# Kernel tuning notes

Hardware: AMD Instinct MI355X
Metric: run time of the kernel (lower is better)

## Reference

```python
import jax, jax.numpy as jnp
import numpy as np

NGRAM_NS = (2, 3)  # window sizes of the 2 hidden layers ('2,3,4' -> num_hidden_layers=2)


def _ngram(x, n):
    # x: (b, s, d) -> (b, s, n, d); window i holds x[i:i+n], zero-padded at the end
    s = x.shape[1]
    xp = jnp.pad(x, ((0, 0), (0, n - 1), (0, 0)))
    return jnp.stack([xp[:, j:j + s] for j in range(n)], axis=2)


def _mixture_weighted(r, i, w):
    # r,i: (..., n, d); w: (..., n, 1) -> weighted sum of outer products |phi><phi|
    w = w[..., 0]
    Rr = jnp.einsum('...nd,...ne,...n->...de', r, r, w) + jnp.einsum('...nd,...ne,...n->...de', i, i, w)
    Ri = jnp.einsum('...nd,...ne,...n->...de', i, r, w) - jnp.einsum('...nd,...ne,...n->...de', r, i, w)
    return Rr, Ri


def _normalize_complex(vr, vi):
    n = jnp.sqrt(jnp.sum(vr * vr + vi * vi, axis=-1, keepdims=True))
    return vr / n, vi / n


def _quad_form(Rr, Ri, vr, vi):
    # <v_k| rho |v_k> for each measurement vector v_k; Rr,Ri: (..., d, d); vr,vi: (k, d)
    ar = jnp.einsum('...de,ke->...dk', Rr, vr) - jnp.einsum('...de,ke->...dk', Ri, vi)
    ai = jnp.einsum('...de,ke->...dk', Rr, vi) + jnp.einsum('...de,ke->...dk', Ri, vr)
    out_r = jnp.einsum('kd,...dk->...k', vr, ar) + jnp.einsum('kd,...dk->...k', vi, ai)
    out_i = jnp.einsum('kd,...dk->...k', vr, ai) - jnp.einsum('kd,...dk->...k', vi, ar)
    return out_r, out_i


def setup_inputs() -> dict:
    key = jax.random.key(0)
    ks = jax.random.split(key, 9)
    V, D, B, S, U, L = 50000, 100, 16, 128, 100, 2
    return {
        'input_seq': jax.random.randint(ks[0], (B, S), 0, V),
        'amp_table': jax.random.normal(ks[1], (V, D), jnp.float32),
        'phase_table': jax.random.uniform(ks[2], (V, D), jnp.float32, -np.pi, np.pi),
        'proj_kernel_r': jax.random.normal(ks[3], (L, D, D), jnp.float32),
        'proj_kernel_i': jax.random.normal(ks[4], (L, D, D), jnp.float32),
        'meas_kernel_r': jax.random.normal(ks[5], (U, D), jnp.float32),
        'meas_kernel_i': jax.random.normal(ks[6], (U, D), jnp.float32),
        'dense_w': jax.random.normal(ks[7], (U, 2), jnp.float32) * 0.1,
        'dense_b': jnp.zeros((2,), jnp.float32),
    }


def reference(input_seq, amp_table, phase_table, proj_kernel_r, proj_kernel_i,
              meas_kernel_r, meas_kernel_i, dense_w, dense_b):
    # ComplexEmbedding
    amp = amp_table[input_seq]      # (b, s, d)
    phase = phase_table[input_seq]  # (b, s, d)
    # L2Norm / L2Normalization
    weights = jnp.linalg.norm(amp, axis=-1, keepdims=True)  # (b, s, 1)
    amp = amp / weights
    # ComplexMultiply: state = amp * e^{i phase}
    seq_r = amp * jnp.cos(phase)
    seq_i = amp * jnp.sin(phase)
    for li, n in enumerate(NGRAM_NS):
        gr = _ngram(seq_r, n)                                  # (b, s, n, d)
        gi = _ngram(seq_i, n)
        gw = jax.nn.softmax(_ngram(weights, n), axis=1)        # Softmax(dim=1) as in torch code
        Rr, Ri = _mixture_weighted(gr, gi, gw)                 # (b, s, d, d)
        vr, vi = _normalize_complex(proj_kernel_r[li], proj_kernel_i[li])
        seq_r, seq_i = _quad_form(Rr, Ri, vr, vi)              # (b, s, d)
    # Final mixture over the sequence dim with the raw L2-norm weights
    Rr, Ri = _mixture_weighted(seq_r, seq_i, weights)          # (b, d, d)
    vr, vi = _normalize_complex(meas_kernel_r, meas_kernel_i)
    probs, _ = _quad_form(Rr, Ri, vr, vi)                      # (b, units) real part of Tr(rho P_k)
    return probs @ dense_w + dense_b
```

## Files before the change

### kernel.cpp

```cpp
#include <hip/hip_runtime.h>
#include <math.h>

#define NB 16
#define SS 128
#define DD 100
#define KK 100
#define T_TILE 8
#define P_HALO 11
#define NTILES 16
#define NT 768
#define NWAVES 12
#define CH_D4 5
#define NCHUNK 5

template<int MODE>
__device__ __forceinline__ void accum_slot(
    const float4* __restrict__ vtb,
    const float4 (*__restrict__ bxr)[25], const float4 (*__restrict__ bxi)[25],
    int p, int k, int c, float& ar, float& ai)
{
#pragma unroll
  for (int r = 0; r < CH_D4; ++r) {
    const int d4 = c * CH_D4 + r;
    const float4 vr4 = vtb[r * KK + k];
    const float4 vi4 = vtb[500 + r * KK + k];
    const float4 x4  = bxr[p][d4];
    if (MODE == 0) {
      const float4 z4 = bxi[p][d4];
      ar += vr4.x * x4.x + vr4.y * x4.y + vr4.z * x4.z + vr4.w * x4.w
          + vi4.x * z4.x + vi4.y * z4.y + vi4.z * z4.z + vi4.w * z4.w;
      ai += vr4.x * z4.x + vr4.y * z4.y + vr4.z * z4.z + vr4.w * z4.w
          - vi4.x * x4.x - vi4.y * x4.y - vi4.z * x4.z - vi4.w * x4.w;
    } else {
      ar += vr4.x * x4.x + vr4.y * x4.y + vr4.z * x4.z + vr4.w * x4.w;
      ai += vi4.x * x4.x + vi4.y * x4.y + vi4.z * x4.z + vi4.w * x4.w;
    }
  }
}

template<int MODE>
__device__ __forceinline__ void run_stage(
    const float* __restrict__ gvr, const float* __restrict__ gvi,
    float4 (*__restrict__ vt)[1000],
    const float4 (*__restrict__ bxr)[25], const float4 (*__restrict__ bxi)[25],
    float* __restrict__ mflat, float2* __restrict__ y2flat,
    float* __restrict__ invvn, const int nslots,
    const int tid, const int lane, const int wid)
{
  if (tid < 4 * KK) {
    const int k = tid >> 2, q = tid & 3;
    const float* r0 = gvr + k * DD + q;
    const float* i0 = gvi + k * DD + q;
    float s = 0.f;
#pragma unroll
    for (int i = 0; i < 25; ++i) { const float a = r0[4*i], c2 = i0[4*i]; s += a*a + c2*c2; }
    s += __shfl_xor(s, 1, 64);
    s += __shfl_xor(s, 2, 64);
    if (q == 0) invvn[k] = 1.0f / s;
  }

  const int e0 = tid;
  const int e1 = tid + NT;
  const int p0 = e0 / 500, rm0 = e0 % 500, r0_ = rm0 / 100, k0_ = rm0 % 100;
  const int p1 = e1 / 500, rm1 = e1 % 500, r1_ = rm1 / 100, k1_ = rm1 % 100;
  const float* g0 = (p0 ? gvi : gvr) + k0_ * DD + 4 * r0_;
  const float* g1 = (p1 ? gvi : gvr) + k1_ * DD + 4 * r1_;

  float4 pv0, pv1;
  pv0 = *(const float4*)(g0);
  if (e1 < 1000) pv1 = *(const float4*)(g1);
  vt[0][e0] = pv0;
  if (e1 < 1000) vt[0][e1] = pv1;
  __syncthreads();

  const int s0 = wid, s1 = wid + NWAVES;
  float a0r = 0.f, a0i = 0.f, a1r = 0.f, a1i = 0.f;
  const int kk0 = (s0 & 1) * 50 + lane;
  const int kk1 = (s1 & 1) * 50 + lane;
  const int pp0 = s0 >> 1, pp1 = s1 >> 1;

  for (int c = 0; c < NCHUNK; ++c) {
    const int buf = c & 1;
    if (c + 1 < NCHUNK) {
      pv0 = *(const float4*)(g0 + 4 * CH_D4 * (c + 1));
      if (e1 < 1000) pv1 = *(const float4*)(g1 + 4 * CH_D4 * (c + 1));
    }
    if (lane < 50) {
      if (s0 < nslots) accum_slot<MODE>(vt[buf], bxr, bxi, pp0, kk0, c, a0r, a0i);
      if (s1 < nslots) accum_slot<MODE>(vt[buf], bxr, bxi, pp1, kk1, c, a1r, a1i);
    }
    if (c + 1 < NCHUNK) {
      const int nb = buf ^ 1;
      vt[nb][e0] = pv0;
      if (e1 < 1000) vt[nb][e1] = pv1;
    }
    __syncthreads();
  }

  if (lane < 50) {
    if (s0 < nslots) {
      if (MODE == 0) mflat[pp0 * KK + kk0] = (a0r * a0r + a0i * a0i) * invvn[kk0];
      else           y2flat[pp0 * KK + kk0] = make_float2(a0r, a0i);
    }
    if (s1 < nslots) {
      if (MODE == 0) mflat[pp1 * KK + kk1] = (a1r * a1r + a1i * a1i) * invvn[kk1];
      else           y2flat[pp1 * KK + kk1] = make_float2(a1r, a1i);
    }
  }
}

__global__ __launch_bounds__(NT) void k_fused(
    const int* __restrict__ seq,
    const float* __restrict__ ampT, const float* __restrict__ phT,
    const float* __restrict__ pkr, const float* __restrict__ pki,
    const float* __restrict__ mkr, const float* __restrict__ mki,
    float* __restrict__ part)
{
  __shared__ float4 vt[2][1000];
  __shared__ float4 xr4[P_HALO][25];
  __shared__ float4 xi4[P_HALO][25];
  __shared__ float4 m4[P_HALO][25];
  __shared__ float2 y2[P_HALO][KK];
  __shared__ float es[SS];
  __shared__ float wnl[SS];
  __shared__ float invvn[KK];
  __shared__ float redw[NWAVES];
  __shared__ float sc[3];

  const int tid  = threadIdx.x;
  const int lane = tid & 63;
  const int wid  = tid >> 6;
  const int bt   = blockIdx.x;
  const int b    = bt >> 4;
  const int tile = bt & 15;
  const int t0   = tile * T_TILE;
  const int sb   = b * SS;

  if (tid < 4 * SS) {
    const int t = tid >> 2, q = tid & 3;
    const int row = seq[sb + t];
    const float* ap = ampT + (long)row * DD + q;
    float s = 0.f;
#pragma unroll
    for (int i = 0; i < 25; ++i) { const float a = ap[4*i]; s += a * a; }
    s += __shfl_xor(s, 1, 64);
    s += __shfl_xor(s, 2, 64);
    if (q == 0) { const float nrm = sqrtf(s); wnl[t] = nrm; es[t] = expf(nrm); }
  }
  __syncthreads();

  {
    float v = (tid < SS) ? es[tid] : 0.f;
    for (int m = 32; m; m >>= 1) v += __shfl_xor(v, m, 64);
    if (lane == 0) redw[wid] = v;
  }
  for (int idx = tid; idx < P_HALO * 25; idx += NT) {
    const int p = idx / 25, d4 = idx % 25;
    const int tp = t0 + p;
    float4 o_r = {0.f, 0.f, 0.f, 0.f}, o_i = {0.f, 0.f, 0.f, 0.f};
    if (tp < SS) {
      const int row = seq[sb + tp];
      const float4 a4 = *(const float4*)(ampT + (long)row * DD + 4 * d4);
      const float4 p4 = *(const float4*)(phT  + (long)row * DD + 4 * d4);
      const float inv = 1.0f / wnl[tp];
      float sv, cv;
      sincosf(p4.x, &sv, &cv); o_r.x = a4.x * inv * cv; o_i.x = a4.x * inv * sv;
      sincosf(p4.y, &sv, &cv); o_r.y = a4.y * inv * cv; o_i.y = a4.y * inv * sv;
      sincosf(p4.z, &sv, &cv); o_r.z = a4.z * inv * cv; o_i.z = a4.z * inv * sv;
      sincosf(p4.w, &sv, &cv); o_r.w = a4.w * inv * cv; o_i.w = a4.w * inv * sv;
    }
    xr4[p][d4] = o_r;
    xi4[p][d4] = o_i;
  }
  __syncthreads();
  if (tid == 0) {
    float E = 0.f;
    for (int w = 0; w < NWAVES; ++w) E += redw[w];
    sc[0] = E;
    sc[1] = E - es[0] + 1.0f;
    sc[2] = E - es[0] - es[1] + 2.0f;
  }
  __syncthreads();

  run_stage<0>(pkr, pki, vt, xr4, xi4, (float*)m4, nullptr, invvn,
               2 * P_HALO, tid, lane, wid);
  __syncthreads();

  run_stage<1>(pkr + DD * DD, pki + DD * DD, vt, m4, m4, nullptr,
               (float2*)y2, invvn, 2 * P_HALO, tid, lane, wid);
  __syncthreads();

  {
    const float E = sc[0], Z1 = sc[1];
    for (int idx = tid; idx < 10 * KK; idx += NT) {
      const int p = idx / KK, k = idx - p * KK;
      const int t = t0 + p;
      const float w0 = ((t     < SS) ? es[t]     : 1.f) / E;
      const float w1 = ((t + 1 < SS) ? es[t + 1] : 1.f) / Z1;
      const float2 ya = y2[p][k], yb = y2[p + 1][k];
      const float ar = w0 * ya.x + w1 * yb.x;
      const float ai = w0 * ya.y + w1 * yb.y;
      ((float*)m4)[p * KK + k] = (ar * ar + ai * ai) * invvn[k];
    }
  }
  __syncthreads();

  run_stage<1>(mkr, mki, vt, m4, m4, nullptr,
               (float2*)y2, invvn, 20, tid, lane, wid);
  __syncthreads();

  {
    const float E = sc[0], Z1 = sc[1], Z2 = sc[2];
    for (int idx = tid; idx < T_TILE * KK; idx += NT) {
      const int p = idx / KK, k = idx - p * KK;
      const int t = t0 + p;
      const float w0 = es[t] / E;
      const float w1 = ((t + 1 < SS) ? es[t + 1] : 1.f) / Z1;
      const float w2 = ((t + 2 < SS) ? es[t + 2] : 1.f) / Z2;
      const float2 ya = y2[p][k], yb = y2[p + 1][k], yc = y2[p + 2][k];
      const float qr = w0 * ya.x + w1 * yb.x + w2 * yc.x;
      const float qi = w0 * ya.y + w1 * yb.y + w2 * yc.y;
      ((float*)m4)[p * KK + k] = wnl[t] * (qr * qr + qi * qi) * invvn[k];
    }
  }
  __syncthreads();
  if (tid < KK) {
    float s = 0.f;
#pragma unroll
    for (int p = 0; p < T_TILE; ++p) s += ((float*)m4)[p * KK + tid];
    part[bt * KK + tid] = s;
  }
}

__global__ __launch_bounds__(128) void k_out(
    const float* __restrict__ part, const float* __restrict__ dw,
    const float* __restrict__ db, float* __restrict__ out)
{
  __shared__ float pr[KK];
  const int b = blockIdx.x, tid = threadIdx.x;
  if (tid < KK) {
    float s = 0.f;
#pragma unroll
    for (int q = 0; q < NTILES; ++q) s += part[(b * NTILES + q) * KK + tid];
    pr[tid] = s;
  }
  __syncthreads();
  if (tid < 2) {
    float s = db[tid];
    for (int k = 0; k < KK; ++k) s += pr[k] * dw[k * 2 + tid];
    out[b * 2 + tid] = s;
  }
}

extern "C" void kernel_launch(void* const* d_in, const int* in_sizes, int n_in,
                              void* d_out, int out_size, void* d_ws, size_t ws_size,
                              hipStream_t stream) {
  const int*   seq  = (const int*)d_in[0];
  const float* ampT = (const float*)d_in[1];
  const float* phT  = (const float*)d_in[2];
  const float* pkr  = (const float*)d_in[3];
  const float* pki  = (const float*)d_in[4];
  const float* mkr  = (const float*)d_in[5];
  const float* mki  = (const float*)d_in[6];
  const float* dw   = (const float*)d_in[7];
  const float* db   = (const float*)d_in[8];
  float* out  = (float*)d_out;
  float* part = (float*)d_ws;

  k_fused<<<NB * NTILES, NT, 0, stream>>>(seq, ampT, phT, pkr, pki, mkr, mki, part);
  k_out  <<<NB,          128, 0, stream>>>(part, dw, db, out);
}
```

Baseline: 35.46 us.

## Stage activations in global workspace and read them with wave-uniform scalar loads

Embedded activations and intermediate stage outputs now go to global workspace buffers instead of shared memory. Each wave reads three positions' activation rows through s_load into scalar registers, while lanes hold per-unit vectors from a padded LDS buffer. The projection norm is folded into the accumulation loop, the block shrinks to 512 threads, and the final mixing is reduced straight into the partial sums. The aim is to cut LDS traffic and redundant broadcast reads. In exchange the kernel takes extra global round-trips and relies on scalar-cache visibility of data the same block has just written.

Result: slower. 50.84 us (+43.4%).

```diff
diff --git a/kernel.cpp b/kernel.cpp
--- a/kernel.cpp
+++ b/kernel.cpp
@@ -6,107 +6,157 @@
 #define DD 100
 #define KK 100
 #define T_TILE 8
-#define P_HALO 11
 #define NTILES 16
-#define NT 768
-#define NWAVES 12
-#define CH_D4 5
-#define NCHUNK 5
-
-template<int MODE>
-__device__ __forceinline__ void accum_slot(
-    const float4* __restrict__ vtb,
-    const float4 (*__restrict__ bxr)[25], const float4 (*__restrict__ bxi)[25],
-    int p, int k, int c, float& ar, float& ai)
-{
-#pragma unroll
-  for (int r = 0; r < CH_D4; ++r) {
-    const int d4 = c * CH_D4 + r;
-    const float4 vr4 = vtb[r * KK + k];
-    const float4 vi4 = vtb[500 + r * KK + k];
-    const float4 x4  = bxr[p][d4];
-    if (MODE == 0) {
-      const float4 z4 = bxi[p][d4];
-      ar += vr4.x * x4.x + vr4.y * x4.y + vr4.z * x4.z + vr4.w * x4.w
-          + vi4.x * z4.x + vi4.y * z4.y + vi4.z * z4.z + vi4.w * z4.w;
-      ai += vr4.x * z4.x + vr4.y * z4.y + vr4.z * z4.z + vr4.w * z4.w
-          - vi4.x * x4.x - vi4.y * x4.y - vi4.z * x4.z - vi4.w * x4.w;
-    } else {
-      ar += vr4.x * x4.x + vr4.y * x4.y + vr4.z * x4.z + vr4.w * x4.w;
-      ai += vi4.x * x4.x + vi4.y * x4.y + vi4.z * x4.z + vi4.w * x4.w;
-    }
+#define NT 512
+#define ROWF 112
+#define VSTR 52
+#define VPLANE 5200
+#define XROW(b,t) ((((b) << 7) + (t)) * ROWF)
+
+typedef float sf16 __attribute__((ext_vector_type(16)));
+typedef float sf8  __attribute__((ext_vector_type(8)));
+typedef float sf4  __attribute__((ext_vector_type(4)));
+
+__device__ __forceinline__ sf16 sl16(const float* p) {
+  sf16 r; asm volatile("s_load_dwordx16 %0, %1, 0x0" : "=s"(r) : "s"((unsigned long long)p)); return r;
+}
+__device__ __forceinline__ sf8 sl8(const float* p) {
+  sf8 r; asm volatile("s_load_dwordx8 %0, %1, 0x0" : "=s"(r) : "s"((unsigned long long)p)); return r;
+}
+__device__ __forceinline__ sf4 sl4(const float* p) {
+  sf4 r; asm volatile("s_load_dwordx4 %0, %1, 0x0" : "=s"(r) : "s"((unsigned long long)p)); return r;
+}
+
+template<int NF4>
+__device__ __forceinline__ void vload(const float* __restrict__ sr, const float* __restrict__ si,
+                                      int cd, int tid, float4 (&vr)[6]) {
+  const int tot = 2 * KK * NF4;
+#pragma unroll
+  for (int i = 0; i < 6; ++i) {
+    const int e = tid + i * NT;
+    if (e < tot) {
+      const int part = e / (KK * NF4);
+      const int r = e - part * (KK * NF4);
+      const int k = r / NF4;
+      const int j = r - k * NF4;
+      vr[i] = *(const float4*)((part ? si : sr) + k * DD + cd + 4 * j);
+    }
+  }
+}
+template<int NF4>
+__device__ __forceinline__ void vstore(float* __restrict__ vbuf, int tid, const float4 (&vr)[6]) {
+  const int tot = 2 * KK * NF4;
+#pragma unroll
+  for (int i = 0; i < 6; ++i) {
+    const int e = tid + i * NT;
+    if (e < tot) {
+      const int part = e / (KK * NF4);
+      const int r = e - part * (KK * NF4);
+      const int k = r / NF4;
+      const int j = r - k * NF4;
+      *(float4*)&vbuf[part * VPLANE + k * VSTR + 4 * j] = vr[i];
+    }
+  }
+}
+
+#define NRM() nacc += vr.x*vr.x+vr.y*vr.y+vr.z*vr.z+vr.w*vr.w \
+                    + vi.x*vi.x+vi.y*vi.y+vi.z*vi.z+vi.w*vi.w
+#define C0B(AX, BX, P) \
+  ar[P]+=vr.x*AX[4*u+0]+vr.y*AX[4*u+1]+vr.z*AX[4*u+2]+vr.w*AX[4*u+3] \
+       +vi.x*BX[4*u+0]+vi.y*BX[4*u+1]+vi.z*BX[4*u+2]+vi.w*BX[4*u+3]; \
+  ai[P]+=vr.x*BX[4*u+0]+vr.y*BX[4*u+1]+vr.z*BX[4*u+2]+vr.w*BX[4*u+3] \
+       -vi.x*AX[4*u+0]-vi.y*AX[4*u+1]-vi.z*AX[4*u+2]-vi.w*AX[4*u+3];
+#define C1B(AX, P) \
+  ar[P]+=vr.x*AX[4*u+0]+vr.y*AX[4*u+1]+vr.z*AX[4*u+2]+vr.w*AX[4*u+3]; \
+  ai[P]+=vi.x*AX[4*u+0]+vi.y*AX[4*u+1]+vi.z*AX[4*u+2]+vi.w*AX[4*u+3];
+
+template<int ND4>
+__device__ __forceinline__ void fma_c0(const float* __restrict__ vbuf, int ke,
+    const float* xr0, const float* xr1, const float* xr2,
+    const float* xi0, const float* xi1, const float* xi2,
+    int cd, float (&ar)[3], float (&ai)[3], float& nacc) {
+  const float* vb = vbuf + ke * VSTR;
+#pragma unroll 1
+  for (int s = 0; s < ND4 / 2; ++s) {
+    sf8 a0 = sl8(xr0 + cd + 8*s), a1 = sl8(xr1 + cd + 8*s), a2 = sl8(xr2 + cd + 8*s);
+    sf8 b0 = sl8(xi0 + cd + 8*s), b1 = sl8(xi1 + cd + 8*s), b2 = sl8(xi2 + cd + 8*s);
+    asm volatile("s_waitcnt lgkmcnt(0)"
+                 : "+s"(a0), "+s"(a1), "+s"(a2), "+s"(b0), "+s"(b1), "+s"(b2));
+#pragma unroll
+    for (int u = 0; u < 2; ++u) {
+      const float4 vr = *(const float4*)(vb + (2*s+u)*4);
+      const float4 vi = *(const float4*)(vb + VPLANE + (2*s+u)*4);
+      NRM();
+      C0B(a0, b0, 0) C0B(a1, b1, 1) C0B(a2, b2, 2)
+    }
+  }
+  if (ND4 & 1) {
+    const int off = cd + 8 * (ND4 / 2);
+    sf4 a0 = sl4(xr0 + off), a1 = sl4(xr1 + off), a2 = sl4(xr2 + off);
+    sf4 b0 = sl4(xi0 + off), b1 = sl4(xi1 + off), b2 = sl4(xi2 + off);
+    asm volatile("s_waitcnt lgkmcnt(0)"
+                 : "+s"(a0), "+s"(a1), "+s"(a2), "+s"(b0), "+s"(b1), "+s"(b2));
+    const int u = 0;
+    const float4 vr = *(const float4*)(vb + (ND4-1)*4);
+    const float4 vi = *(const float4*)(vb + VPLANE + (ND4-1)*4);
+    NRM();
+    C0B(a0, b0, 0) C0B(a1, b1, 1) C0B(a2, b2, 2)
+  }
+}
+
+template<int ND4>
+__device__ __forceinline__ void fma_c1(const float* __restrict__ vbuf, int ke,
+    const float* x0, const float* x1, const float* x2,
+    int cd, float (&ar)[3], float (&ai)[3], float& nacc) {
+  const float* vb = vbuf + ke * VSTR;
+#pragma unroll 1
+  for (int s = 0; s < ND4 / 4; ++s) {
+    sf16 a0 = sl16(x0 + cd + 16*s), a1 = sl16(x1 + cd + 16*s), a2 = sl16(x2 + cd + 16*s);
+    asm volatile("s_waitcnt lgkmcnt(0)" : "+s"(a0), "+s"(a1), "+s"(a2));
+#pragma unroll
+    for (int u = 0; u < 4; ++u) {
+      const float4 vr = *(const float4*)(vb + (4*s+u)*4);
+      const float4 vi = *(const float4*)(vb + VPLANE + (4*s+u)*4);
+      NRM();
+      C1B(a0, 0) C1B(a1, 1) C1B(a2, 2)
+    }
+  }
+  if (ND4 & 3) {
+    const int off = cd + 16 * (ND4 / 4);
+    sf4 a0 = sl4(x0 + off), a1 = sl4(x1 + off), a2 = sl4(x2 + off);
+    asm volatile("s_waitcnt lgkmcnt(0)" : "+s"(a0), "+s"(a1), "+s"(a2));
+    const int u = 0;
+    const float4 vr = *(const float4*)(vb + (ND4-1)*4);
+    const float4 vi = *(const float4*)(vb + VPLANE + (ND4-1)*4);
+    NRM();
+    C1B(a0, 0) C1B(a1, 1) C1B(a2, 2)
   }
 }
 
 template<int MODE>
 __device__ __forceinline__ void run_stage(
     const float* __restrict__ gvr, const float* __restrict__ gvi,
-    float4 (*__restrict__ vt)[1000],
-    const float4 (*__restrict__ bxr)[25], const float4 (*__restrict__ bxi)[25],
-    float* __restrict__ mflat, float2* __restrict__ y2flat,
-    float* __restrict__ invvn, const int nslots,
-    const int tid, const int lane, const int wid)
-{
-  if (tid < 4 * KK) {
-    const int k = tid >> 2, q = tid & 3;
-    const float* r0 = gvr + k * DD + q;
-    const float* i0 = gvi + k * DD + q;
-    float s = 0.f;
-#pragma unroll
-    for (int i = 0; i < 25; ++i) { const float a = r0[4*i], c2 = i0[4*i]; s += a*a + c2*c2; }
-    s += __shfl_xor(s, 1, 64);
-    s += __shfl_xor(s, 2, 64);
-    if (q == 0) invvn[k] = 1.0f / s;
-  }
-
-  const int e0 = tid;
-  const int e1 = tid + NT;
-  const int p0 = e0 / 500, rm0 = e0 % 500, r0_ = rm0 / 100, k0_ = rm0 % 100;
-  const int p1 = e1 / 500, rm1 = e1 % 500, r1_ = rm1 / 100, k1_ = rm1 % 100;
-  const float* g0 = (p0 ? gvi : gvr) + k0_ * DD + 4 * r0_;
-  const float* g1 = (p1 ? gvi : gvr) + k1_ * DD + 4 * r1_;
-
-  float4 pv0, pv1;
-  pv0 = *(const float4*)(g0);
-  if (e1 < 1000) pv1 = *(const float4*)(g1);
-  vt[0][e0] = pv0;
-  if (e1 < 1000) vt[0][e1] = pv1;
-  __syncthreads();
-
-  const int s0 = wid, s1 = wid + NWAVES;
-  float a0r = 0.f, a0i = 0.f, a1r = 0.f, a1i = 0.f;
-  const int kk0 = (s0 & 1) * 50 + lane;
-  const int kk1 = (s1 & 1) * 50 + lane;
-  const int pp0 = s0 >> 1, pp1 = s1 >> 1;
-
-  for (int c = 0; c < NCHUNK; ++c) {
-    const int buf = c & 1;
-    if (c + 1 < NCHUNK) {
-      pv0 = *(const float4*)(g0 + 4 * CH_D4 * (c + 1));
-      if (e1 < 1000) pv1 = *(const float4*)(g1 + 4 * CH_D4 * (c + 1));
-    }
-    if (lane < 50) {
-      if (s0 < nslots) accum_slot<MODE>(vt[buf], bxr, bxi, pp0, kk0, c, a0r, a0i);
-      if (s1 < nslots) accum_slot<MODE>(vt[buf], bxr, bxi, pp1, kk1, c, a1r, a1i);
-    }
-    if (c + 1 < NCHUNK) {
-      const int nb = buf ^ 1;
-      vt[nb][e0] = pv0;
-      if (e1 < 1000) vt[nb][e1] = pv1;
-    }
-    __syncthreads();
-  }
-
-  if (lane < 50) {
-    if (s0 < nslots) {
-      if (MODE == 0) mflat[pp0 * KK + kk0] = (a0r * a0r + a0i * a0i) * invvn[kk0];
-      else           y2flat[pp0 * KK + kk0] = make_float2(a0r, a0i);
-    }
-    if (s1 < nslots) {
-      if (MODE == 0) mflat[pp1 * KK + kk1] = (a1r * a1r + a1i * a1i) * invvn[kk1];
-      else           y2flat[pp1 * KK + kk1] = make_float2(a1r, a1i);
-    }
-  }
+    const float* xr0, const float* xr1, const float* xr2,
+    const float* xi0, const float* xi1, const float* xi2,
+    float* __restrict__ vbuf, float* __restrict__ invvn,
+    int tid, int ke, bool nwrite, float (&ar)[3], float (&ai)[3]) {
+  float4 vreg[6];
+  ar[0] = ar[1] = ar[2] = 0.f; ai[0] = ai[1] = ai[2] = 0.f;
+  float nacc = 0.f;
+  vload<12>(gvr, gvi, 0, tid, vreg);
+  vstore<12>(vbuf, tid, vreg);
+  __syncthreads();
+  vload<13>(gvr, gvi, 48, tid, vreg);
+  if (MODE == 0) fma_c0<12>(vbuf, ke, xr0, xr1, xr2, xi0, xi1, xi2, 0, ar, ai, nacc);
+  else           fma_c1<12>(vbuf, ke, xr0, xr1, xr2, 0, ar, ai, nacc);
+  __syncthreads();
+  vstore<13>(vbuf, tid, vreg);
+  __syncthreads();
+  if (MODE == 0) fma_c0<13>(vbuf, ke, xr0, xr1, xr2, xi0, xi1, xi2, 48, ar, ai, nacc);
+  else           fma_c1<13>(vbuf, ke, xr0, xr1, xr2, 48, ar, ai, nacc);
+  __syncthreads();
+  if (nwrite) invvn[ke] = 1.0f / nacc;
+  __syncthreads();
 }
 
 __global__ __launch_bounds__(NT) void k_fused(
@@ -114,134 +164,166 @@
     const float* __restrict__ ampT, const float* __restrict__ phT,
     const float* __restrict__ pkr, const float* __restrict__ pki,
     const float* __restrict__ mkr, const float* __restrict__ mki,
-    float* __restrict__ part)
-{
-  __shared__ float4 vt[2][1000];
-  __shared__ float4 xr4[P_HALO][25];
-  __shared__ float4 xi4[P_HALO][25];
-  __shared__ float4 m4[P_HALO][25];
-  __shared__ float2 y2[P_HALO][KK];
-  __shared__ float es[SS];
-  __shared__ float wnl[SS];
-  __shared__ float invvn[KK];
-  __shared__ float redw[NWAVES];
-  __shared__ float sc[3];
+    float* __restrict__ PR, float* __restrict__ PI,
+    float* __restrict__ M1, float* __restrict__ M2,
+    float* __restrict__ part) {
+  __shared__ float vbuf[2 * VPLANE];
+  __shared__ float2 y2l[11 * 102];
+  __shared__ float es[SS], wnl[SS], invvn[KK];
+  __shared__ float redw[2], sc[3];
 
   const int tid  = threadIdx.x;
   const int lane = tid & 63;
-  const int wid  = tid >> 6;
+  const int wid  = __builtin_amdgcn_readfirstlane(tid >> 6);
   const int bt   = blockIdx.x;
   const int b    = bt >> 4;
-  const int tile = bt & 15;
-  const int t0   = tile * T_TILE;
+  const int t0   = (bt & 15) * T_TILE;
   const int sb   = b * SS;
-
-  if (tid < 4 * SS) {
-    const int t = tid >> 2, q = tid & 3;
+  const int q    = wid & 1;
+  const int pg   = wid >> 1;
+  const int ke   = q * 50 + (lane < 50 ? lane : 49);
+  const int pp0 = pg, pp1 = pg + 4, pp2 = pg + 8;
+
+  {
+    const int t = tid >> 2, qq = tid & 3;
     const int row = seq[sb + t];
-    const float* ap = ampT + (long)row * DD + q;
+    const float* ap = ampT + (long)row * DD + qq;
     float s = 0.f;
 #pragma unroll
     for (int i = 0; i < 25; ++i) { const float a = ap[4*i]; s += a * a; }
-    s += __shfl_xor(s, 1, 64);
-    s += __shfl_xor(s, 2, 64);
-    if (q == 0) { const float nrm = sqrtf(s); wnl[t] = nrm; es[t] = expf(nrm); }
-  }
-  __syncthreads();
-
+    s += __shfl_xor(s, 1); s += __shfl_xor(s, 2);
+    if (qq == 0) { const float n = sqrtf(s); wnl[t] = n; es[t] = expf(n); }
+  }
+  __syncthreads();
   {
     float v = (tid < SS) ? es[tid] : 0.f;
-    for (int m = 32; m; m >>= 1) v += __shfl_xor(v, m, 64);
-    if (lane == 0) redw[wid] = v;
-  }
-  for (int idx = tid; idx < P_HALO * 25; idx += NT) {
-    const int p = idx / 25, d4 = idx % 25;
-    const int tp = t0 + p;
-    float4 o_r = {0.f, 0.f, 0.f, 0.f}, o_i = {0.f, 0.f, 0.f, 0.f};
-    if (tp < SS) {
-      const int row = seq[sb + tp];
-      const float4 a4 = *(const float4*)(ampT + (long)row * DD + 4 * d4);
-      const float4 p4 = *(const float4*)(phT  + (long)row * DD + 4 * d4);
-      const float inv = 1.0f / wnl[tp];
-      float sv, cv;
-      sincosf(p4.x, &sv, &cv); o_r.x = a4.x * inv * cv; o_i.x = a4.x * inv * sv;
-      sincosf(p4.y, &sv, &cv); o_r.y = a4.y * inv * cv; o_i.y = a4.y * inv * sv;
-      sincosf(p4.z, &sv, &cv); o_r.z = a4.z * inv * cv; o_i.z = a4.z * inv * sv;
-      sincosf(p4.w, &sv, &cv); o_r.w = a4.w * inv * cv; o_i.w = a4.w * inv * sv;
-    }
-    xr4[p][d4] = o_r;
-    xi4[p][d4] = o_i;
+    if (tid < SS) {
+      for (int m = 32; m; m >>= 1) v += __shfl_xor(v, m);
+      if (lane == 0) redw[tid >> 6] = v;
+    }
+  }
+  for (int e = tid; e < 11 * DD; e += NT) {
+    const int p = e / DD, d = e - p * DD;
+    const int t = t0 + p;
+    if (t < SS) {
+      const int row = seq[sb + t];
+      const float a  = ampT[(long)row * DD + d];
+      const float ph = phT[(long)row * DD + d];
+      float sv, cv; sincosf(ph, &sv, &cv);
+      const float an = a / wnl[t];
+      PR[XROW(b, t) + d] = an * cv;
+      PI[XROW(b, t) + d] = an * sv;
+    }
   }
   __syncthreads();
   if (tid == 0) {
-    float E = 0.f;
-    for (int w = 0; w < NWAVES; ++w) E += redw[w];
-    sc[0] = E;
-    sc[1] = E - es[0] + 1.0f;
-    sc[2] = E - es[0] - es[1] + 2.0f;
-  }
-  __syncthreads();
-
-  run_stage<0>(pkr, pki, vt, xr4, xi4, (float*)m4, nullptr, invvn,
-               2 * P_HALO, tid, lane, wid);
-  __syncthreads();
-
-  run_stage<1>(pkr + DD * DD, pki + DD * DD, vt, m4, m4, nullptr,
-               (float2*)y2, invvn, 2 * P_HALO, tid, lane, wid);
-  __syncthreads();
-
-  {
-    const float E = sc[0], Z1 = sc[1];
+    const float E = redw[0] + redw[1];
+    sc[0] = E; sc[1] = E - es[0] + 1.0f; sc[2] = E - es[0] - es[1] + 2.0f;
+  }
+  __syncthreads();
+
+  float ar[3], ai[3];
+  const bool nwr = (wid < 2) && (lane < 63 ? (lane < 50) : false);
+
+  {
+    const int r0 = min(t0 + min(pp0, 10), SS - 1);
+    const int r1 = min(t0 + min(pp1, 10), SS - 1);
+    const int r2 = min(t0 + min(pp2, 10), SS - 1);
+    run_stage<0>(pkr, pki,
+                 PR + XROW(b, r0), PR + XROW(b, r1), PR + XROW(b, r2),
+                 PI + XROW(b, r0), PI + XROW(b, r1), PI + XROW(b, r2),
+                 vbuf, invvn, tid, ke, nwr, ar, ai);
+#pragma unroll
+    for (int j = 0; j < 3; ++j) {
+      const int pp = pg + 4 * j;
+      const int t = t0 + pp;
+      if (pp < 11 && t < SS && lane < 50)
+        M1[XROW(b, t) + ke] = (ar[j] * ar[j] + ai[j] * ai[j]) * invvn[ke];
+    }
+    __syncthreads();
+  }
+
+  {
+    const int r0 = min(t0 + min(pp0, 10), SS - 1);
+    const int r1 = min(t0 + min(pp1, 10), SS - 1);
+    const int r2 = min(t0 + min(pp2, 10), SS - 1);
+    run_stage<1>(pkr + DD * DD, pki + DD * DD,
+                 M1 + XROW(b, r0), M1 + XROW(b, r1), M1 + XROW(b, r2),
+                 nullptr, nullptr, nullptr,
+                 vbuf, invvn, tid, ke, nwr, ar, ai);
+#pragma unroll
+    for (int j = 0; j < 3; ++j) {
+      const int pp = pg + 4 * j;
+      if (pp < 11 && lane < 50) y2l[pp * 102 + ke] = make_float2(ar[j], ai[j]);
+    }
+    __syncthreads();
     for (int idx = tid; idx < 10 * KK; idx += NT) {
       const int p = idx / KK, k = idx - p * KK;
       const int t = t0 + p;
-      const float w0 = ((t     < SS) ? es[t]     : 1.f) / E;
-      const float w1 = ((t + 1 < SS) ? es[t + 1] : 1.f) / Z1;
-      const float2 ya = y2[p][k], yb = y2[p + 1][k];
-      const float ar = w0 * ya.x + w1 * yb.x;
-      const float ai = w0 * ya.y + w1 * yb.y;
-      ((float*)m4)[p * KK + k] = (ar * ar + ai * ai) * invvn[k];
-    }
-  }
-  __syncthreads();
-
-  run_stage<1>(mkr, mki, vt, m4, m4, nullptr,
-               (float2*)y2, invvn, 20, tid, lane, wid);
-  __syncthreads();
-
-  {
-    const float E = sc[0], Z1 = sc[1], Z2 = sc[2];
-    for (int idx = tid; idx < T_TILE * KK; idx += NT) {
-      const int p = idx / KK, k = idx - p * KK;
-      const int t = t0 + p;
-      const float w0 = es[t] / E;
-      const float w1 = ((t + 1 < SS) ? es[t + 1] : 1.f) / Z1;
-      const float w2 = ((t + 2 < SS) ? es[t + 2] : 1.f) / Z2;
-      const float2 ya = y2[p][k], yb = y2[p + 1][k], yc = y2[p + 2][k];
-      const float qr = w0 * ya.x + w1 * yb.x + w2 * yc.x;
-      const float qi = w0 * ya.y + w1 * yb.y + w2 * yc.y;
-      ((float*)m4)[p * KK + k] = wnl[t] * (qr * qr + qi * qi) * invvn[k];
-    }
-  }
-  __syncthreads();
-  if (tid < KK) {
-    float s = 0.f;
-#pragma unroll
-    for (int p = 0; p < T_TILE; ++p) s += ((float*)m4)[p * KK + tid];
-    part[bt * KK + tid] = s;
+      if (t < SS) {
+        const float w0 = es[t] / sc[0];
+        float qr = w0 * y2l[p * 102 + k].x;
+        float qi = w0 * y2l[p * 102 + k].y;
+        if (t + 1 < SS) {
+          const float w1 = es[t + 1] / sc[1];
+          qr += w1 * y2l[(p + 1) * 102 + k].x;
+          qi += w1 * y2l[(p + 1) * 102 + k].y;
+        }
+        M2[XROW(b, t) + k] = (qr * qr + qi * qi) * invvn[k];
+      }
+    }
+    __syncthreads();
+  }
+
+  {
+    const int r0 = min(t0 + min(pp0, 9), SS - 1);
+    const int r1 = min(t0 + min(pp1, 9), SS - 1);
+    const int r2 = min(t0 + min(pp2, 9), SS - 1);
+    run_stage<1>(mkr, mki,
+                 M2 + XROW(b, r0), M2 + XROW(b, r1), M2 + XROW(b, r2),
+                 nullptr, nullptr, nullptr,
+                 vbuf, invvn, tid, ke, nwr, ar, ai);
+#pragma unroll
+    for (int j = 0; j < 3; ++j) {
+      const int pp = pg + 4 * j;
+      if (pp < 10 && lane < 50) y2l[pp * 102 + ke] = make_float2(ar[j], ai[j]);
+    }
+    __syncthreads();
+    if (tid < KK) {
+      const int k = tid;
+      float accf = 0.f;
+#pragma unroll
+      for (int p = 0; p < T_TILE; ++p) {
+        const int t = t0 + p;
+        const float w0 = es[t] / sc[0];
+        float qr = w0 * y2l[p * 102 + k].x;
+        float qi = w0 * y2l[p * 102 + k].y;
+        if (t + 1 < SS) {
+          const float w1 = es[t + 1] / sc[1];
+          qr += w1 * y2l[(p + 1) * 102 + k].x;
+          qi += w1 * y2l[(p + 1) * 102 + k].y;
+        }
+        if (t + 2 < SS) {
+          const float w2 = es[t + 2] / sc[2];
+          qr += w2 * y2l[(p + 2) * 102 + k].x;
+          qi += w2 * y2l[(p + 2) * 102 + k].y;
+        }
+        accf += wnl[t] * (qr * qr + qi * qi);
+      }
+      part[bt * KK + k] = accf * invvn[k];
+    }
   }
 }
 
 __global__ __launch_bounds__(128) void k_out(
     const float* __restrict__ part, const float* __restrict__ dw,
-    const float* __restrict__ db, float* __restrict__ out)
-{
+    const float* __restrict__ db, float* __restrict__ out) {
   __shared__ float pr[KK];
   const int b = blockIdx.x, tid = threadIdx.x;
   if (tid < KK) {
     float s = 0.f;
 #pragma unroll
-    for (int q = 0; q < NTILES; ++q) s += part[(b * NTILES + q) * KK + tid];
+    for (int qq = 0; qq < NTILES; ++qq) s += part[(b * NTILES + qq) * KK + tid];
     pr[tid] = s;
   }
   __syncthreads();
@@ -264,9 +346,17 @@
   const float* mki  = (const float*)d_in[6];
   const float* dw   = (const float*)d_in[7];
   const float* db   = (const float*)d_in[8];
-  float* out  = (float*)d_out;
-  float* part = (float*)d_ws;
-
-  k_fused<<<NB * NTILES, NT, 0, stream>>>(seq, ampT, phT, pkr, pki, mkr, mki, part);
+  float* out = (float*)d_out;
+
+  float* ws = (float*)d_ws;
+  const int R = NB * SS * ROWF;
+  float* PR   = ws;
+  float* PI   = ws + R;
+  float* M1   = ws + 2 * R;
+  float* M2   = ws + 3 * R;
+  float* part = ws + 4 * R;
+
+  k_fused<<<NB * NTILES, NT, 0, stream>>>(seq, ampT, phT, pkr, pki, mkr, mki,
+                                          PR, PI, M1, M2, part);
   k_out  <<<NB,          128, 0, stream>>>(part, dw, db, out);
 }
```

## Hold measurement vectors in registers and split D across waves with partial sums

Applied to the files above, without the earlier changes.

Each stage now has every thread load its slice of two measurement vectors straight from global memory into registers. A thread covers 4 positions, and the d dimension is split across 4 wave groups whose partial sums are reduced through shared memory. This removes the double-buffered LDS staging of the whole projection matrix and its per-chunk barriers, and computes norms inline. The in-between weighting steps are folded into the stage epilogues, and the final reduction is fused. The cost is more registers per thread (launch bounds set to 3 blocks) and extra LDS traffic for the partial-sum reduction.

After: 37.85 us. 6.8% more time.

```diff
diff --git a/kernel.cpp b/kernel.cpp
--- a/kernel.cpp
+++ b/kernel.cpp
@@ -6,234 +6,282 @@
 #define DD 100
 #define KK 100
 #define T_TILE 8
-#define P_HALO 11
 #define NTILES 16
 #define NT 768
-#define NWAVES 12
-#define CH_D4 5
-#define NCHUNK 5
-
-template<int MODE>
-__device__ __forceinline__ void accum_slot(
-    const float4* __restrict__ vtb,
-    const float4 (*__restrict__ bxr)[25], const float4 (*__restrict__ bxi)[25],
-    int p, int k, int c, float& ar, float& ai)
+
+__device__ __forceinline__ float dot4(const float4 a, const float4 b) {
+  return a.x * b.x + a.y * b.y + a.z * b.z + a.w * b.w;
+}
+
+template<int MODE, int CM, int NA, int NB2>
+__device__ __forceinline__ void do_stage(
+    const float* __restrict__ gvr, const float* __restrict__ gvi,
+    const float4 (*__restrict__ xR)[25], const float4 (*__restrict__ xI)[25],
+    float4 (*__restrict__ partl)[11][50],
+    float2 (*__restrict__ nrmh)[50],
+    float* __restrict__ mdst, float2* __restrict__ y3f,
+    float* __restrict__ invvnU,
+    const float* __restrict__ es, const float* __restrict__ sc,
+    int df4, int pmaxF, int pmaxC,
+    int k0, bool act, int g, int h, int t0)
 {
-#pragma unroll
-  for (int r = 0; r < CH_D4; ++r) {
-    const int d4 = c * CH_D4 + r;
-    const float4 vr4 = vtb[r * KK + k];
-    const float4 vi4 = vtb[500 + r * KK + k];
-    const float4 x4  = bxr[p][d4];
-    if (MODE == 0) {
-      const float4 z4 = bxi[p][d4];
-      ar += vr4.x * x4.x + vr4.y * x4.y + vr4.z * x4.z + vr4.w * x4.w
-          + vi4.x * z4.x + vi4.y * z4.y + vi4.z * z4.z + vi4.w * z4.w;
-      ai += vr4.x * z4.x + vr4.y * z4.y + vr4.z * z4.z + vr4.w * z4.w
-          - vi4.x * x4.x - vi4.y * x4.y - vi4.z * x4.z - vi4.w * x4.w;
-    } else {
-      ar += vr4.x * x4.x + vr4.y * x4.y + vr4.z * x4.z + vr4.w * x4.w;
-      ai += vi4.x * x4.x + vi4.y * x4.y + vi4.z * x4.z + vi4.w * x4.w;
-    }
-  }
-}
-
-template<int MODE>
-__device__ __forceinline__ void run_stage(
-    const float* __restrict__ gvr, const float* __restrict__ gvi,
-    float4 (*__restrict__ vt)[1000],
-    const float4 (*__restrict__ bxr)[25], const float4 (*__restrict__ bxi)[25],
-    float* __restrict__ mflat, float2* __restrict__ y2flat,
-    float* __restrict__ invvn, const int nslots,
-    const int tid, const int lane, const int wid)
-{
-  if (tid < 4 * KK) {
-    const int k = tid >> 2, q = tid & 3;
-    const float* r0 = gvr + k * DD + q;
-    const float* i0 = gvi + k * DD + q;
-    float s = 0.f;
-#pragma unroll
-    for (int i = 0; i < 25; ++i) { const float a = r0[4*i], c2 = i0[4*i]; s += a*a + c2*c2; }
-    s += __shfl_xor(s, 1, 64);
-    s += __shfl_xor(s, 2, 64);
-    if (q == 0) invvn[k] = 1.0f / s;
-  }
-
-  const int e0 = tid;
-  const int e1 = tid + NT;
-  const int p0 = e0 / 500, rm0 = e0 % 500, r0_ = rm0 / 100, k0_ = rm0 % 100;
-  const int p1 = e1 / 500, rm1 = e1 % 500, r1_ = rm1 / 100, k1_ = rm1 % 100;
-  const float* g0 = (p0 ? gvi : gvr) + k0_ * DD + 4 * r0_;
-  const float* g1 = (p1 ? gvi : gvr) + k1_ * DD + 4 * r1_;
-
-  float4 pv0, pv1;
-  pv0 = *(const float4*)(g0);
-  if (e1 < 1000) pv1 = *(const float4*)(g1);
-  vt[0][e0] = pv0;
-  if (e1 < 1000) vt[0][e1] = pv1;
-  __syncthreads();
-
-  const int s0 = wid, s1 = wid + NWAVES;
-  float a0r = 0.f, a0i = 0.f, a1r = 0.f, a1i = 0.f;
-  const int kk0 = (s0 & 1) * 50 + lane;
-  const int kk1 = (s1 & 1) * 50 + lane;
-  const int pp0 = s0 >> 1, pp1 = s1 >> 1;
-
-  for (int c = 0; c < NCHUNK; ++c) {
-    const int buf = c & 1;
-    if (c + 1 < NCHUNK) {
-      pv0 = *(const float4*)(g0 + 4 * CH_D4 * (c + 1));
-      if (e1 < 1000) pv1 = *(const float4*)(g1 + 4 * CH_D4 * (c + 1));
-    }
-    if (lane < 50) {
-      if (s0 < nslots) accum_slot<MODE>(vt[buf], bxr, bxi, pp0, kk0, c, a0r, a0i);
-      if (s1 < nslots) accum_slot<MODE>(vt[buf], bxr, bxi, pp1, kk1, c, a1r, a1i);
-    }
-    if (c + 1 < NCHUNK) {
-      const int nb = buf ^ 1;
-      vt[nb][e0] = pv0;
-      if (e1 < 1000) vt[nb][e1] = pv1;
-    }
-    __syncthreads();
-  }
-
-  if (lane < 50) {
-    if (s0 < nslots) {
-      if (MODE == 0) mflat[pp0 * KK + kk0] = (a0r * a0r + a0i * a0i) * invvn[kk0];
-      else           y2flat[pp0 * KK + kk0] = make_float2(a0r, a0i);
-    }
-    if (s1 < nslots) {
-      if (MODE == 0) mflat[pp1 * KK + kk1] = (a1r * a1r + a1i * a1i) * invvn[kk1];
-      else           y2flat[pp1 * KK + kk1] = make_float2(a1r, a1i);
-    }
-  }
-}
-
-__global__ __launch_bounds__(NT) void k_fused(
+  const float* vr0 = gvr + k0 * DD + 4 * df4;
+  const float* vi0 = gvi + k0 * DD + 4 * df4;
+  float acr[4][2] = {{0.f,0.f},{0.f,0.f},{0.f,0.f},{0.f,0.f}};
+  float aci[4][2] = {{0.f,0.f},{0.f,0.f},{0.f,0.f},{0.f,0.f}};
+  float n0 = 0.f, n1 = 0.f;
+
+  {
+    float4 V[NA][2][2];
+#pragma unroll
+    for (int j = 0; j < NA; ++j) {
+      V[j][0][0] = *(const float4*)(vr0 + 4 * j);
+      V[j][1][0] = *(const float4*)(vr0 + DD + 4 * j);
+      V[j][0][1] = *(const float4*)(vi0 + 4 * j);
+      V[j][1][1] = *(const float4*)(vi0 + DD + 4 * j);
+    }
+#pragma unroll
+    for (int j = 0; j < NA; ++j) {
+      n0 += dot4(V[j][0][0], V[j][0][0]) + dot4(V[j][0][1], V[j][0][1]);
+      n1 += dot4(V[j][1][0], V[j][1][0]) + dot4(V[j][1][1], V[j][1][1]);
+    }
+#pragma unroll
+    for (int e = 0; e < 4; ++e) {
+      const int p = 4 * g + e;
+      if (p <= pmaxF) {
+        const float4* xrow  = &xR[p][df4];
+        const float4* xirow = &xI[p][df4];
+#pragma unroll
+        for (int j = 0; j < NA; ++j) {
+          const float4 xr = xrow[j];
+          if (MODE == 0) {
+            const float4 xi = xirow[j];
+            acr[e][0] += dot4(V[j][0][0], xr) + dot4(V[j][0][1], xi);
+            aci[e][0] += dot4(V[j][0][0], xi) - dot4(V[j][0][1], xr);
+            acr[e][1] += dot4(V[j][1][0], xr) + dot4(V[j][1][1], xi);
+            aci[e][1] += dot4(V[j][1][0], xi) - dot4(V[j][1][1], xr);
+          } else {
+            acr[e][0] += dot4(V[j][0][0], xr);
+            aci[e][0] += dot4(V[j][0][1], xr);
+            acr[e][1] += dot4(V[j][1][0], xr);
+            aci[e][1] += dot4(V[j][1][1], xr);
+          }
+        }
+      }
+    }
+  }
+  {
+    float4 V[NB2][2][2];
+#pragma unroll
+    for (int j = 0; j < NB2; ++j) {
+      V[j][0][0] = *(const float4*)(vr0 + 4 * (NA + j));
+      V[j][1][0] = *(const float4*)(vr0 + DD + 4 * (NA + j));
+      V[j][0][1] = *(const float4*)(vi0 + 4 * (NA + j));
+      V[j][1][1] = *(const float4*)(vi0 + DD + 4 * (NA + j));
+    }
+#pragma unroll
+    for (int j = 0; j < NB2; ++j) {
+      n0 += dot4(V[j][0][0], V[j][0][0]) + dot4(V[j][0][1], V[j][0][1]);
+      n1 += dot4(V[j][1][0], V[j][1][0]) + dot4(V[j][1][1], V[j][1][1]);
+    }
+#pragma unroll
+    for (int e = 0; e < 4; ++e) {
+      const int p = 4 * g + e;
+      if (p <= pmaxF) {
+        const float4* xrow  = &xR[p][df4 + NA];
+        const float4* xirow = &xI[p][df4 + NA];
+#pragma unroll
+        for (int j = 0; j < NB2; ++j) {
+          const float4 xr = xrow[j];
+          if (MODE == 0) {
+            const float4 xi = xirow[j];
+            acr[e][0] += dot4(V[j][0][0], xr) + dot4(V[j][0][1], xi);
+            aci[e][0] += dot4(V[j][0][0], xi) - dot4(V[j][0][1], xr);
+            acr[e][1] += dot4(V[j][1][0], xr) + dot4(V[j][1][1], xi);
+            aci[e][1] += dot4(V[j][1][0], xi) - dot4(V[j][1][1], xr);
+          } else {
+            acr[e][0] += dot4(V[j][0][0], xr);
+            aci[e][0] += dot4(V[j][0][1], xr);
+            acr[e][1] += dot4(V[j][1][0], xr);
+            aci[e][1] += dot4(V[j][1][1], xr);
+          }
+        }
+      }
+    }
+  }
+
+  const int kp = k0 >> 1;
+  if (act) {
+#pragma unroll
+    for (int e = 0; e < 4; ++e) {
+      const int p = 4 * g + e;
+      if (p <= pmaxF)
+        partl[h][p][kp] = make_float4(acr[e][0], aci[e][0], acr[e][1], aci[e][1]);
+    }
+    if (g == 0) nrmh[h][kp] = make_float2(n0, n1);
+  }
+  __syncthreads();
+
+  if (h == 0 && act) {
+    const float2 q0 = nrmh[0][kp], q1 = nrmh[1][kp], q2 = nrmh[2][kp], q3 = nrmh[3][kp];
+    const float iv0 = 1.f / (q0.x + q1.x + q2.x + q3.x);
+    const float iv1 = 1.f / (q0.y + q1.y + q2.y + q3.y);
+#pragma unroll
+    for (int e = 0; e < 4; ++e) {
+      const int p = 4 * g + e;
+      if (p <= pmaxC) {
+        float4 s  = partl[0][p][kp];
+        float4 b1 = partl[1][p][kp], b2 = partl[2][p][kp], b3 = partl[3][p][kp];
+        s.x += b1.x + b2.x + b3.x;  s.y += b1.y + b2.y + b3.y;
+        s.z += b1.z + b2.z + b3.z;  s.w += b1.w + b2.w + b3.w;
+        if (CM == 1) {
+          *(float2*)(mdst + p * 100 + k0) =
+              make_float2((s.x * s.x + s.y * s.y) * iv0,
+                          (s.z * s.z + s.w * s.w) * iv1);
+        } else if (CM == 2) {
+          float4 u  = partl[0][p + 1][kp];
+          float4 c1 = partl[1][p + 1][kp], c2 = partl[2][p + 1][kp], c3 = partl[3][p + 1][kp];
+          u.x += c1.x + c2.x + c3.x;  u.y += c1.y + c2.y + c3.y;
+          u.z += c1.z + c2.z + c3.z;  u.w += c1.w + c2.w + c3.w;
+          const int t = t0 + p;
+          const float w0 = es[t] / sc[0];
+          const float w1 = es[t + 1] / sc[1];
+          const float r0 = w0 * s.x + w1 * u.x, i0 = w0 * s.y + w1 * u.y;
+          const float r1 = w0 * s.z + w1 * u.z, i1 = w0 * s.w + w1 * u.w;
+          *(float2*)(mdst + p * 100 + k0) =
+              make_float2((r0 * r0 + i0 * i0) * iv0, (r1 * r1 + i1 * i1) * iv1);
+        } else {
+          *(float4*)(y3f + p * 100 + k0) = s;
+        }
+      }
+    }
+    if (CM == 3 && g == 0) { invvnU[k0] = iv0; invvnU[k0 + 1] = iv1; }
+  }
+  __syncthreads();
+}
+
+__global__ __launch_bounds__(NT, 3) void k_fused(
     const int* __restrict__ seq,
     const float* __restrict__ ampT, const float* __restrict__ phT,
     const float* __restrict__ pkr, const float* __restrict__ pki,
     const float* __restrict__ mkr, const float* __restrict__ mki,
-    float* __restrict__ part)
+    float* __restrict__ partg)
 {
-  __shared__ float4 vt[2][1000];
-  __shared__ float4 xr4[P_HALO][25];
-  __shared__ float4 xi4[P_HALO][25];
-  __shared__ float4 m4[P_HALO][25];
-  __shared__ float2 y2[P_HALO][KK];
-  __shared__ float es[SS];
+  __shared__ float4 xbR[11][25];
+  __shared__ float4 xbI[11][25];
+  __shared__ float4 partl[4][11][50];
+  __shared__ float2 y3[10][100];
+  __shared__ float2 nrmh[4][50];
+  __shared__ float invvnU[KK];
+  __shared__ float es[SS + 8];
   __shared__ float wnl[SS];
-  __shared__ float invvn[KK];
-  __shared__ float redw[NWAVES];
+  __shared__ float redw[2];
   __shared__ float sc[3];
 
   const int tid  = threadIdx.x;
   const int lane = tid & 63;
   const int wid  = tid >> 6;
+  const int h    = wid & 3;
+  const int g    = wid >> 2;
+  const bool act = lane < 50;
+  const int kp   = act ? lane : 49;
+  const int k0   = 2 * kp;
+  const int df4  = (h == 0) ? 0 : 7 + 6 * (h - 1);
   const int bt   = blockIdx.x;
   const int b    = bt >> 4;
-  const int tile = bt & 15;
-  const int t0   = tile * T_TILE;
+  const int t0   = (bt & 15) * T_TILE;
   const int sb   = b * SS;
 
-  if (tid < 4 * SS) {
-    const int t = tid >> 2, q = tid & 3;
+  if (tid < 512) {
+    const int t = tid >> 2, qq = tid & 3;
     const int row = seq[sb + t];
-    const float* ap = ampT + (long)row * DD + q;
+    const float* ap = ampT + (long)row * DD;
     float s = 0.f;
 #pragma unroll
-    for (int i = 0; i < 25; ++i) { const float a = ap[4*i]; s += a * a; }
-    s += __shfl_xor(s, 1, 64);
-    s += __shfl_xor(s, 2, 64);
-    if (q == 0) { const float nrm = sqrtf(s); wnl[t] = nrm; es[t] = expf(nrm); }
-  }
-  __syncthreads();
-
-  {
-    float v = (tid < SS) ? es[tid] : 0.f;
-    for (int m = 32; m; m >>= 1) v += __shfl_xor(v, m, 64);
-    if (lane == 0) redw[wid] = v;
-  }
-  for (int idx = tid; idx < P_HALO * 25; idx += NT) {
-    const int p = idx / 25, d4 = idx % 25;
-    const int tp = t0 + p;
-    float4 o_r = {0.f, 0.f, 0.f, 0.f}, o_i = {0.f, 0.f, 0.f, 0.f};
-    if (tp < SS) {
-      const int row = seq[sb + tp];
-      const float4 a4 = *(const float4*)(ampT + (long)row * DD + 4 * d4);
-      const float4 p4 = *(const float4*)(phT  + (long)row * DD + 4 * d4);
-      const float inv = 1.0f / wnl[tp];
-      float sv, cv;
-      sincosf(p4.x, &sv, &cv); o_r.x = a4.x * inv * cv; o_i.x = a4.x * inv * sv;
-      sincosf(p4.y, &sv, &cv); o_r.y = a4.y * inv * cv; o_i.y = a4.y * inv * sv;
-      sincosf(p4.z, &sv, &cv); o_r.z = a4.z * inv * cv; o_i.z = a4.z * inv * sv;
-      sincosf(p4.w, &sv, &cv); o_r.w = a4.w * inv * cv; o_i.w = a4.w * inv * sv;
-    }
-    xr4[p][d4] = o_r;
-    xi4[p][d4] = o_i;
+    for (int i = 0; i < 7; ++i) {
+      const int j = qq + 4 * i;
+      if (j < 25) {
+        const float4 a = *(const float4*)(ap + 4 * j);
+        s += a.x * a.x + a.y * a.y + a.z * a.z + a.w * a.w;
+      }
+    }
+    s += __shfl_xor(s, 1);
+    s += __shfl_xor(s, 2);
+    if (qq == 0) { const float n = sqrtf(s); wnl[t] = n; es[t] = expf(n); }
+  }
+  if (tid >= 512 && tid < 520) es[SS + tid - 512] = 0.f;
+  __syncthreads();
+
+  if (tid < SS) {
+    float v = es[tid];
+#pragma unroll
+    for (int m = 32; m; m >>= 1) v += __shfl_xor(v, m);
+    if ((tid & 63) == 0) redw[tid >> 6] = v;
+  }
+  for (int e2 = tid; e2 < 11 * DD; e2 += NT) {
+    const int p = e2 / DD, d = e2 - p * DD;
+    const int t = t0 + p;
+    float pr = 0.f, pi = 0.f;
+    if (t < SS) {
+      const int row = seq[sb + t];
+      const float a  = ampT[(long)row * DD + d];
+      const float ph = phT[(long)row * DD + d];
+      float sv, cv; sincosf(ph, &sv, &cv);
+      const float an = a / wnl[t];
+      pr = an * cv; pi = an * sv;
+    }
+    ((float*)xbR)[p * 100 + d] = pr;
+    ((float*)xbI)[p * 100 + d] = pi;
   }
   __syncthreads();
   if (tid == 0) {
-    float E = 0.f;
-    for (int w = 0; w < NWAVES; ++w) E += redw[w];
-    sc[0] = E;
-    sc[1] = E - es[0] + 1.0f;
-    sc[2] = E - es[0] - es[1] + 2.0f;
-  }
-  __syncthreads();
-
-  run_stage<0>(pkr, pki, vt, xr4, xi4, (float*)m4, nullptr, invvn,
-               2 * P_HALO, tid, lane, wid);
-  __syncthreads();
-
-  run_stage<1>(pkr + DD * DD, pki + DD * DD, vt, m4, m4, nullptr,
-               (float2*)y2, invvn, 2 * P_HALO, tid, lane, wid);
-  __syncthreads();
-
-  {
-    const float E = sc[0], Z1 = sc[1];
-    for (int idx = tid; idx < 10 * KK; idx += NT) {
-      const int p = idx / KK, k = idx - p * KK;
+    const float E = redw[0] + redw[1];
+    sc[0] = E; sc[1] = E - es[0] + 1.f; sc[2] = E - es[0] - es[1] + 2.f;
+  }
+  __syncthreads();
+
+  if (h == 0) do_stage<0,1,4,3>(pkr, pki, xbR, xbI, partl, nrmh,
+                                (float*)xbR, nullptr, invvnU, es, sc,
+                                0,   10, 10, k0, act, g, h, t0);
+  else        do_stage<0,1,3,3>(pkr, pki, xbR, xbI, partl, nrmh,
+                                (float*)xbR, nullptr, invvnU, es, sc,
+                                df4, 10, 10, k0, act, g, h, t0);
+
+  if (h == 0) do_stage<1,2,4,3>(pkr + DD * DD, pki + DD * DD, xbR, xbI, partl, nrmh,
+                                (float*)xbI, nullptr, invvnU, es, sc,
+                                0,   10, 9, k0, act, g, h, t0);
+  else        do_stage<1,2,3,3>(pkr + DD * DD, pki + DD * DD, xbR, xbI, partl, nrmh,
+                                (float*)xbI, nullptr, invvnU, es, sc,
+                                df4, 10, 9, k0, act, g, h, t0);
+
+  if (h == 0) do_stage<1,3,4,3>(mkr, mki, xbI, xbI, partl, nrmh,
+                                nullptr, (float2*)y3, invvnU, es, sc,
+                                0,   9, 9, k0, act, g, h, t0);
+  else        do_stage<1,3,3,3>(mkr, mki, xbI, xbI, partl, nrmh,
+                                nullptr, (float2*)y3, invvnU, es, sc,
+                                df4, 9, 9, k0, act, g, h, t0);
+
+  if (tid < KK) {
+    const int k = tid;
+    const float iE = 1.f / sc[0], iZ1 = 1.f / sc[1], iZ2 = 1.f / sc[2];
+    float acc = 0.f;
+#pragma unroll
+    for (int p = 0; p < T_TILE; ++p) {
       const int t = t0 + p;
-      const float w0 = ((t     < SS) ? es[t]     : 1.f) / E;
-      const float w1 = ((t + 1 < SS) ? es[t + 1] : 1.f) / Z1;
-      const float2 ya = y2[p][k], yb = y2[p + 1][k];
-      const float ar = w0 * ya.x + w1 * yb.x;
-      const float ai = w0 * ya.y + w1 * yb.y;
-      ((float*)m4)[p * KK + k] = (ar * ar + ai * ai) * invvn[k];
-    }
-  }
-  __syncthreads();
-
-  run_stage<1>(mkr, mki, vt, m4, m4, nullptr,
-               (float2*)y2, invvn, 20, tid, lane, wid);
-  __syncthreads();
-
-  {
-    const float E = sc[0], Z1 = sc[1], Z2 = sc[2];
-    for (int idx = tid; idx < T_TILE * KK; idx += NT) {
-      const int p = idx / KK, k = idx - p * KK;
-      const int t = t0 + p;
-      const float w0 = es[t] / E;
-      const float w1 = ((t + 1 < SS) ? es[t + 1] : 1.f) / Z1;
-      const float w2 = ((t + 2 < SS) ? es[t + 2] : 1.f) / Z2;
-      const float2 ya = y2[p][k], yb = y2[p + 1][k], yc = y2[p + 2][k];
-      const float qr = w0 * ya.x + w1 * yb.x + w2 * yc.x;
-      const float qi = w0 * ya.y + w1 * yb.y + w2 * yc.y;
-      ((float*)m4)[p * KK + k] = wnl[t] * (qr * qr + qi * qi) * invvn[k];
-    }
-  }
-  __syncthreads();
-  if (tid < KK) {
-    float s = 0.f;
-#pragma unroll
-    for (int p = 0; p < T_TILE; ++p) s += ((float*)m4)[p * KK + tid];
-    part[bt * KK + tid] = s;
+      const float w0 = es[t] * iE;
+      const float w1 = es[t + 1] * iZ1;
+      const float w2 = es[t + 2] * iZ2;
+      const float2 a = y3[p][k], bb = y3[p + 1][k], c = y3[p + 2][k];
+      const float qr = w0 * a.x + w1 * bb.x + w2 * c.x;
+      const float qi = w0 * a.y + w1 * bb.y + w2 * c.y;
+      acc += wnl[t] * (qr * qr + qi * qi);
+    }
+    partg[bt * KK + k] = acc * invvnU[k];
   }
 }
 
 __global__ __launch_bounds__(128) void k_out(
-    const float* __restrict__ part, const float* __restrict__ dw,
+    const float* __restrict__ partg, const float* __restrict__ dw,
     const float* __restrict__ db, float* __restrict__ out)
 {
   __shared__ float pr[KK];
@@ -241,7 +289,7 @@
   if (tid < KK) {
     float s = 0.f;
 #pragma unroll
-    for (int q = 0; q < NTILES; ++q) s += part[(b * NTILES + q) * KK + tid];
+    for (int q = 0; q < NTILES; ++q) s += partg[(b * NTILES + q) * KK + tid];
     pr[tid] = s;
   }
   __syncthreads();
@@ -264,9 +312,9 @@
   const float* mki  = (const float*)d_in[6];
   const float* dw   = (const float*)d_in[7];
   const float* db   = (const float*)d_in[8];
-  float* out  = (float*)d_out;
-  float* part = (float*)d_ws;
-
-  k_fused<<<NB * NTILES, NT, 0, stream>>>(seq, ampT, phT, pkr, pki, mkr, mki, part);
-  k_out  <<<NB,          128, 0, stream>>>(part, dw, db, out);
-}
+  float* out   = (float*)d_out;
+  float* partg = (float*)d_ws;
+
+  k_fused<<<NB * NTILES, NT, 0, stream>>>(seq, ampT, phT, pkr, pki, mkr, mki, partg);
+  k_out  <<<NB,          128, 0, stream>>>(partg, dw, db, out);
+}
```
